# Kernel optimization log

Measured on AMD Instinct MI355X. Metric: run time of the kernel, lower is better.

## Reference

```python
import jax, jax.numpy as jnp
import numpy as np

B, T, C, H, DH, L, V = 4096, 32, 384, 6, 64, 6, 80


def _ln(x, g, b):
    m = x.mean(-1, keepdims=True)
    v = ((x - m) ** 2).mean(-1, keepdims=True)
    return (x - m) / jnp.sqrt(v + 1e-5) * g + b


def setup_inputs() -> dict:
    key = jax.random.key(0)
    ks = jax.random.split(key, 12)
    n = lambda k, s: jax.random.normal(k, s, dtype=jnp.float32) * 0.02
    return dict(
        idx=jax.random.randint(ks[0], (B, T), 0, V),
        tok_emb=n(ks[1], (V, C)),
        pos_emb=n(ks[2], (T, C)),
        ln1_g=jnp.ones((L, C), jnp.float32), ln1_b=jnp.zeros((L, C), jnp.float32),
        Wq=n(ks[3], (L, H, C, DH)), Wk=n(ks[4], (L, H, C, DH)), Wv=n(ks[5], (L, H, C, DH)),
        Wo=n(ks[6], (L, C, C)), bo=jnp.zeros((L, C), jnp.float32),
        ln2_g=jnp.ones((L, C), jnp.float32), ln2_b=jnp.zeros((L, C), jnp.float32),
        W1=n(ks[7], (L, C, 4 * C)), b1=jnp.zeros((L, 4 * C), jnp.float32),
        W2=n(ks[8], (L, 4 * C, C)), b2=jnp.zeros((L, C), jnp.float32),
        lnf_g=jnp.ones((C,), jnp.float32), lnf_b=jnp.zeros((C,), jnp.float32),
        Wlm=n(ks[9], (C, V)), blm=jnp.zeros((V,), jnp.float32),
    )


def reference(idx, tok_emb, pos_emb, ln1_g, ln1_b, Wq, Wk, Wv, Wo, bo,
              ln2_g, ln2_b, W1, b1, W2, b2, lnf_g, lnf_b, Wlm, blm):
    # token + position embeddings
    x = tok_emb[idx] + pos_emb[None]  # [B, T, C]
    mask = jnp.tril(jnp.ones((T, T), dtype=bool))  # causal

    def block(x, p):
        l1g, l1b, wq, wk, wv, wo, b_o, l2g, l2b, w1, b_1, w2, b_2 = p
        h = _ln(x, l1g, l1b)
        q = jnp.einsum('btc,hcd->bhtd', h, wq)
        k = jnp.einsum('btc,hcd->bhtd', h, wk)
        v = jnp.einsum('btc,hcd->bhtd', h, wv)
        s = jnp.einsum('bhtd,bhsd->bhts', q, k) * (DH ** -0.5)
        s = jnp.where(mask, s, -jnp.inf)
        a = jax.nn.softmax(s, axis=-1)  # dropout is identity in eval
        o = jnp.einsum('bhts,bhsd->bhtd', a, v)
        o = o.transpose(0, 2, 1, 3).reshape(x.shape[0], T, C)  # concat heads
        x = x + o @ wo + b_o
        h2 = _ln(x, l2g, l2b)
        x = x + jax.nn.relu(h2 @ w1 + b_1) @ w2 + b_2
        return x, None

    params = (ln1_g, ln1_b, Wq, Wk, Wv, Wo, bo, ln2_g, ln2_b, W1, b1, W2, b2)
    x, _ = jax.lax.scan(block, x, params)
    x = _ln(x, lnf_g, lnf_b)
    return x @ Wlm + blm  # [B, T, V]
```

## Files before the change

### kernel.cpp

```cpp
#include <hip/hip_runtime.h>
#include <hip/hip_fp16.h>
#include <stdint.h>


typedef unsigned short u16;
typedef __bf16 bf16x8 __attribute__((ext_vector_type(8)));
typedef float f32x4 __attribute__((ext_vector_type(4)));
typedef float f32x4v __attribute__((ext_vector_type(4)));
typedef unsigned uint2v __attribute__((ext_vector_type(2)));

#define M_TOK 131072
#define CDIM  384
#define TT    32
#define HH    6
#define DHEAD 64
#define LLAY  6
#define VOCAB 80
#define FFDIM 1536
#define QKVN  1152

__device__ __forceinline__ float b2f(u16 v) {
    union { unsigned int u; float f; } x; x.u = ((unsigned int)v) << 16; return x.f;
}
__device__ __forceinline__ u16 f2b(float f) {
    union { float f; unsigned int u; } x; x.f = f;
    unsigned int r = (x.u + 0x7fffu + ((x.u >> 16) & 1u)) >> 16;
    return (u16)r;
}
__device__ __forceinline__ void gload16(const u16* g, u16* l) {
    __builtin_amdgcn_global_load_lds(
        (const __attribute__((address_space(1))) void*)g,
        (__attribute__((address_space(3))) void*)l,
        16, 0, 0);
}
__device__ __forceinline__ float load_in(const void* p, size_t i, int m) {
    if (m == 0) return ((const float*)p)[i];
    u16 v = ((const u16*)p)[i];
    if (m == 1) return b2f(v);
    __half h; *(u16*)&h = v; return __half2float(h);
}

__global__ void detect_dtype_kernel(const void* ln1g, int* flag) {
    if (threadIdx.x == 0 && blockIdx.x == 0) {
        unsigned w = *(const unsigned*)ln1g;
        int m = 0;
        if (w == 0x3F803F80u) m = 1;
        else if (w == 0x3C003C00u) m = 2;
        *flag = m;
    }
}

__global__ void cvt_kernel(const void* __restrict__ src, u16* __restrict__ dst,
                           unsigned n, const int* __restrict__ flag) {
    const int m = *flag;
    unsigned i = blockIdx.x * 256 + threadIdx.x;
    if (i < n) dst[i] = f2b(load_in(src, i, m));
}

__global__ void transpose_kernel(const void* __restrict__ src, u16* __restrict__ dst,
                                 int R, int Cc, unsigned total,
                                 const int* __restrict__ flag) {
    const int m = *flag;
    unsigned i = blockIdx.x * 256 + threadIdx.x;
    if (i >= total) return;
    unsigned c  = i % R;
    unsigned t2 = i / R;
    unsigned n  = t2 % Cc;
    unsigned l  = t2 / Cc;
    dst[i] = f2b(load_in(src, ((size_t)l * R + c) * Cc + n, m));
}

__global__ void pack_qkv_kernel(const void* __restrict__ Wq, const void* __restrict__ Wk,
                                const void* __restrict__ Wv, u16* __restrict__ dst,
                                const int* __restrict__ flag) {
    const int m = *flag;
    unsigned i = blockIdx.x * 256 + threadIdx.x;
    const unsigned total = (unsigned)LLAY * QKVN * CDIM;
    if (i >= total) return;
    unsigned c  = i % CDIM;
    unsigned t2 = i / CDIM;
    unsigned n  = t2 % QKVN;
    unsigned l  = t2 / QKVN;
    const void* W = (n < 384) ? Wq : (n < 768) ? Wk : Wv;
    unsigned nn = n % 384;
    unsigned hh = nn >> 6, d = nn & 63;
    dst[i] = f2b(load_in(W, (((size_t)l * HH + hh) * CDIM + c) * DHEAD + d, m));
}

__global__ void embed_kernel(const int* __restrict__ idx, const void* __restrict__ tok,
                             const void* __restrict__ pos, float* __restrict__ x,
                             unsigned rows0, const int* __restrict__ flag) {
    const int m = *flag;
    unsigned i = blockIdx.x * 256 + threadIdx.x;
    unsigned c  = i % CDIM;
    unsigned bt = i / CDIM + rows0;
    unsigned t  = bt & (TT - 1);
    int id = idx[bt];
    x[i] = load_in(tok, (size_t)id * CDIM + c, m) + load_in(pos, (size_t)t * CDIM + c, m);
}

__global__ __launch_bounds__(256) void ln_kernel(const float* __restrict__ x,
                                                 const u16* __restrict__ g,
                                                 const u16* __restrict__ b,
                                                 u16* __restrict__ out) {
    const unsigned row  = blockIdx.x * 4 + (threadIdx.x >> 6);
    const unsigned lane = threadIdx.x & 63;
    const float* xr = x + (size_t)row * CDIM;
    float v[6]; float s = 0.f, s2 = 0.f;
#pragma unroll
    for (int j = 0; j < 6; j++) { v[j] = xr[lane + j * 64]; s += v[j]; s2 += v[j] * v[j]; }
#pragma unroll
    for (int off = 32; off; off >>= 1) { s += __shfl_xor(s, off); s2 += __shfl_xor(s2, off); }
    float mean = s * (1.f / CDIM);
    float var  = fmaxf(s2 * (1.f / CDIM) - mean * mean, 0.f);
    float rstd = rsqrtf(var + 1e-5f);
    u16* orow = out + (size_t)row * CDIM;
#pragma unroll
    for (int j = 0; j < 6; j++) {
        unsigned c = lane + j * 64;
        orow[c] = f2b((v[j] - mean) * rstd * b2f(g[c]) + b2f(b[c]));
    }
}

template<bool BIAS, bool RELU, bool RESID, bool NBOUND, bool FOUT>
__global__ __launch_bounds__(256, 4)
void gemm_kernel(const u16* __restrict__ A, const u16* __restrict__ Bt,
                 const u16* __restrict__ bias, const float* resid,
                 u16* __restrict__ Cb, float* Cf,
                 int N, int K, int nt) {
    __shared__ __align__(16) u16 smem[16384];
    u16* As = smem;
    u16* Bs = smem + 8192;
    float* eps = (float*)smem;

    const int tid  = threadIdx.x;
    const int lane = tid & 63;
    const int w    = tid >> 6;
    const int quad = lane >> 4;
    const int l16  = lane & 15;
    const int wm = w >> 1, wn = w & 1;

    const int id = blockIdx.x;
    const int sgrp = id >> 3;
    const int mtile = (id & 7) + 8 * (sgrp / nt);
    const int ntile = sgrp % nt;
    const long m0 = (long)mtile * 128;
    const long n0 = (long)ntile * 128;

    const u16* Ag[4]; const u16* Bg[4];
    u16* ldsA[4]; u16* ldsB[4];
#pragma unroll
    for (int n = 0; n < 4; n++) {
        const int si  = w * 256 + n * 64 + lane;
        const int row = si >> 3;
        const int p   = si & 7;
        const int s   = p ^ (row & 7);
        Ag[n] = A + (size_t)(m0 + row) * K + s * 8;
        long brow = n0 + row;
        if (NBOUND) brow = brow < N ? brow : N - 1;
        Bg[n] = Bt + (size_t)brow * K + s * 8;
        ldsA[n] = As + (size_t)(w * 256 + n * 64) * 8;
        ldsB[n] = Bs + (size_t)(w * 256 + n * 64) * 8;
    }

    f32x4 acc[4][4];
#pragma unroll
    for (int i = 0; i < 4; i++)
#pragma unroll
        for (int j = 0; j < 4; j++) acc[i][j] = f32x4{0.f, 0.f, 0.f, 0.f};

    for (int k0 = 0; k0 < K; k0 += 64) {
        __syncthreads();
#pragma unroll
        for (int n = 0; n < 4; n++) gload16(Ag[n] + k0, ldsA[n]);
#pragma unroll
        for (int n = 0; n < 4; n++) gload16(Bg[n] + k0, ldsB[n]);
        __syncthreads();
#pragma unroll
        for (int k32 = 0; k32 < 2; k32++) {
            bf16x8 af[4], bfr[4];
#pragma unroll
            for (int i = 0; i < 4; i++) {
                const int row = wm * 64 + i * 16 + l16;
                const int p   = (k32 * 4 + quad) ^ (row & 7);
                af[i] = *(const bf16x8*)(&As[row * 64 + p * 8]);
            }
#pragma unroll
            for (int j = 0; j < 4; j++) {
                const int row = wn * 64 + j * 16 + l16;
                const int p   = (k32 * 4 + quad) ^ (row & 7);
                bfr[j] = *(const bf16x8*)(&Bs[row * 64 + p * 8]);
            }
#pragma unroll
            for (int i = 0; i < 4; i++)
#pragma unroll
                for (int j = 0; j < 4; j++)
                    acc[i][j] = __builtin_amdgcn_mfma_f32_16x16x32_bf16(af[i], bfr[j], acc[i][j], 0, 0, 0);
        }
    }

    float bv[4];
#pragma unroll
    for (int j = 0; j < 4; j++) {
        if (BIAS) {
            int col = (int)n0 + wn * 64 + j * 16 + l16;
            bv[j] = (!NBOUND || col < N) ? b2f(bias[col]) : 0.f;
        } else bv[j] = 0.f;
    }

#pragma unroll
    for (int hhf = 0; hhf < 2; hhf++) {
        __syncthreads();
        if (wm == hhf) {
#pragma unroll
            for (int i = 0; i < 4; i++)
#pragma unroll
                for (int j = 0; j < 4; j++) {
                    const int lr = i * 16 + quad * 4;
                    const int lc = wn * 64 + j * 16 + l16;
#pragma unroll
                    for (int r = 0; r < 4; r++) {
                        float v = acc[i][j][r] + bv[j];
                        if (RELU) v = fmaxf(v, 0.f);
                        eps[(lr + r) * 128 + lc] = v;
                    }
                }
        }
        __syncthreads();
        const long rowbase = m0 + hhf * 64;
        const int lrow0 = tid >> 5;
        const int c = (tid & 31) * 4;
#pragma unroll
        for (int p = 0; p < 8; p++) {
            const int lrow = p * 8 + lrow0;
            const long grow = rowbase + lrow;
            f32x4v v = *(const f32x4v*)&eps[lrow * 128 + c];
            if (RESID) {
                const f32x4v rv = *(const f32x4v*)&resid[grow * N + n0 + c];
                v = v + rv;
                __builtin_nontemporal_store(v, (f32x4v*)&Cf[grow * N + n0 + c]);
            } else if (FOUT) {
                if (!NBOUND || (int)n0 + c + 3 < N)
                    __builtin_nontemporal_store(v, (f32x4v*)&Cf[grow * N + n0 + c]);
            } else {
                if (!NBOUND || (int)n0 + c + 3 < N) {
                    uint2v pk;
                    pk.x = (unsigned)f2b(v.x) | ((unsigned)f2b(v.y) << 16);
                    pk.y = (unsigned)f2b(v.z) | ((unsigned)f2b(v.w) << 16);
                    __builtin_nontemporal_store(pk, (uint2v*)&Cb[grow * N + n0 + c]);
                }
            }
        }
    }
}

__global__ __launch_bounds__(256, 2) void attn_kernel(const u16* __restrict__ qkv,
                                                      u16* __restrict__ o) {
    __shared__ __align__(16) u16 alds[4 * 3840];
    const int w    = threadIdx.x >> 6;
    u16* Pl = alds + w * 3840;
    u16* VT = Pl + 1280;

    const int gw   = blockIdx.x * 4 + w;
    const int seq  = gw / HH;
    const int h    = gw - seq * HH;
    const int lane = threadIdx.x & 63;
    const int l16  = lane & 15;
    const int quad = lane >> 4;

    const u16* base = qkv + (size_t)seq * TT * QKVN;
    const u16* Qb = base + h * DHEAD;
    const u16* Kb = base + 384 + h * DHEAD;
    const u16* Vb = base + 768 + h * DHEAD;

    {
        const int s  = lane & 31;
        const int hf = lane >> 5;
#pragma unroll
        for (int c = 0; c < 4; c++) {
            uint4 v = *(const uint4*)(Vb + (size_t)s * QKVN + hf * 32 + c * 8);
            const u16* pv = (const u16*)&v;
#pragma unroll
            for (int j = 0; j < 8; j++) {
                const int d = hf * 32 + c * 8 + j;
                VT[d * 40 + s] = pv[j];
            }
        }
    }

    bf16x8 qf[2][2], kf[2][2];
#pragma unroll
    for (int ti = 0; ti < 2; ti++)
#pragma unroll
        for (int kt = 0; kt < 2; kt++)
            qf[ti][kt] = *(const bf16x8*)(Qb + (size_t)(ti * 16 + l16) * QKVN + kt * 32 + quad * 8);
#pragma unroll
    for (int si = 0; si < 2; si++)
#pragma unroll
        for (int kt = 0; kt < 2; kt++)
            kf[si][kt] = *(const bf16x8*)(Kb + (size_t)(si * 16 + l16) * QKVN + kt * 32 + quad * 8);

    f32x4 S00 = f32x4{0.f, 0.f, 0.f, 0.f};
    f32x4 S10 = f32x4{0.f, 0.f, 0.f, 0.f};
    f32x4 S11 = f32x4{0.f, 0.f, 0.f, 0.f};
#pragma unroll
    for (int kt = 0; kt < 2; kt++) {
        S00 = __builtin_amdgcn_mfma_f32_16x16x32_bf16(qf[0][kt], kf[0][kt], S00, 0, 0, 0);
        S10 = __builtin_amdgcn_mfma_f32_16x16x32_bf16(qf[1][kt], kf[0][kt], S10, 0, 0, 0);
        S11 = __builtin_amdgcn_mfma_f32_16x16x32_bf16(qf[1][kt], kf[1][kt], S11, 0, 0, 0);
    }

#pragma unroll
    for (int ti = 0; ti < 2; ti++) {
#pragma unroll
        for (int r = 0; r < 4; r++) {
            const int t = ti * 16 + quad * 4 + r;
            float v0 = (ti ? S10[r] : S00[r]) * 0.125f;
            if (l16 > t) v0 = -1e30f;
            float v1 = -1e30f;
            if (ti == 1) {
                v1 = S11[r] * 0.125f;
                if (16 + l16 > t) v1 = -1e30f;
            }
            float m = fmaxf(v0, v1);
#pragma unroll
            for (int k = 1; k < 16; k <<= 1) m = fmaxf(m, __shfl_xor(m, k));
            const float e0 = __expf(v0 - m);
            const float e1 = (ti == 1) ? __expf(v1 - m) : 0.f;
            float l = e0 + e1;
#pragma unroll
            for (int k = 1; k < 16; k <<= 1) l += __shfl_xor(l, k);
            const float inv = 1.f / l;
            Pl[t * 40 + l16]      = f2b(e0 * inv);
            Pl[t * 40 + 16 + l16] = f2b(e1 * inv);
        }
    }

    bf16x8 pf[2], vf[4];
#pragma unroll
    for (int ti = 0; ti < 2; ti++)
        pf[ti] = *(const bf16x8*)(&Pl[(ti * 16 + l16) * 40 + quad * 8]);
#pragma unroll
    for (int dt = 0; dt < 4; dt++)
        vf[dt] = *(const bf16x8*)(&VT[(dt * 16 + l16) * 40 + quad * 8]);

    u16* ob = o + ((size_t)seq * TT) * CDIM + h * DHEAD;
#pragma unroll
    for (int ti = 0; ti < 2; ti++) {
#pragma unroll
        for (int dt = 0; dt < 4; dt++) {
            f32x4 O2 = f32x4{0.f, 0.f, 0.f, 0.f};
            O2 = __builtin_amdgcn_mfma_f32_16x16x32_bf16(pf[ti], vf[dt], O2, 0, 0, 0);
#pragma unroll
            for (int r = 0; r < 4; r++) {
                const int t = ti * 16 + quad * 4 + r;
                ob[(size_t)t * CDIM + dt * 16 + l16] = f2b(O2[r]);
            }
        }
    }
}

extern "C" void kernel_launch(void* const* d_in, const int* in_sizes, int n_in,
                              void* d_out, int out_size, void* d_ws, size_t ws_size,
                              hipStream_t stream) {
    const int*  idx  = (const int*)d_in[0];
    const void* tok  = d_in[1];
    const void* pos  = d_in[2];
    const void* ln1g = d_in[3];
    const void* ln1b = d_in[4];
    const void* Wq   = d_in[5];
    const void* Wk   = d_in[6];
    const void* Wv   = d_in[7];
    const void* Wo   = d_in[8];
    const void* bo   = d_in[9];
    const void* ln2g = d_in[10];
    const void* ln2b = d_in[11];
    const void* W1   = d_in[12];
    const void* b1   = d_in[13];
    const void* W2   = d_in[14];
    const void* b2   = d_in[15];
    const void* lnfg = d_in[16];
    const void* lnfb = d_in[17];
    const void* Wlm  = d_in[18];
    const void* blm  = d_in[19];

    const size_t wq_b  = (size_t)LLAY * QKVN * CDIM * 2;
    const size_t wo_b  = (size_t)LLAY * CDIM * CDIM * 2;
    const size_t w1_b  = (size_t)LLAY * FFDIM * CDIM * 2;
    const size_t w2_b  = (size_t)LLAY * CDIM * FFDIM * 2;
    const size_t wlm_b = (size_t)VOCAB * CDIM * 2;
    const size_t wts   = wq_b + wo_b + w1_b + w2_b + wlm_b;

    const unsigned P_LN1G = 0,      P_LN1B = 2304,  P_BO  = 4608;
    const unsigned P_LN2G = 6912,   P_LN2B = 9216,  P_B1  = 11520;
    const unsigned P_B2   = 20736,  P_LNFG = 23040, P_LNFB = 23424;
    const unsigned P_BLM  = 23808,  P_TOT  = 23888;
    const size_t pbuf_b = ((size_t)P_TOT * 2 + 255) & ~(size_t)255;

    int NC = 32;
    {
        const int cand[6] = {1, 2, 4, 8, 16, 32};
        for (int ci = 0; ci < 6; ci++) {
            size_t rows_c = (size_t)M_TOK / cand[ci];
            size_t need = rows_c * 5376 + wts + pbuf_b + 4096;
            if (need <= ws_size) { NC = cand[ci]; break; }
        }
    }
    const size_t rows = (size_t)M_TOK / NC;
    const int mt = (int)(rows / 128);

    char* ws = (char*)d_ws;
    size_t off = 0;
    float* x    = (float*)(ws + off); off += rows * CDIM * 4;
    u16*   h    = (u16*)(ws + off);   off += rows * CDIM * 2;
    char*  S    = ws + off;           off += rows * 3072;
    u16*   qkv  = (u16*)S;
    u16*   o    = (u16*)(S + rows * QKVN * 2);
    u16*   u    = (u16*)S;
    u16* wqkvT  = (u16*)(ws + off);   off += wq_b;
    u16* woT    = (u16*)(ws + off);   off += wo_b;
    u16* w1T    = (u16*)(ws + off);   off += w1_b;
    u16* w2T    = (u16*)(ws + off);   off += w2_b;
    u16* wlmT   = (u16*)(ws + off);   off += wlm_b;
    u16* pbuf   = (u16*)(ws + off);   off += pbuf_b;
    int* flag   = (int*)(ws + off);   off += 256;

    detect_dtype_kernel<<<1, 64, 0, stream>>>(ln1g, flag);

    struct { const void* src; unsigned doff, n; } cv[10] = {
        { ln1g, P_LN1G, 2304 }, { ln1b, P_LN1B, 2304 }, { bo, P_BO, 2304 },
        { ln2g, P_LN2G, 2304 }, { ln2b, P_LN2B, 2304 }, { b1, P_B1, 9216 },
        { b2,   P_B2,   2304 }, { lnfg, P_LNFG, 384 },  { lnfb, P_LNFB, 384 },
        { blm,  P_BLM,  80 },
    };
    for (int i = 0; i < 10; i++)
        cvt_kernel<<<(cv[i].n + 255) / 256, 256, 0, stream>>>(cv[i].src, pbuf + cv[i].doff, cv[i].n, flag);

    {
        unsigned tq = (unsigned)LLAY * QKVN * CDIM;
        pack_qkv_kernel<<<(tq + 255) / 256, 256, 0, stream>>>(Wq, Wk, Wv, wqkvT, flag);
        unsigned t1 = (unsigned)LLAY * CDIM * CDIM;
        transpose_kernel<<<(t1 + 255) / 256, 256, 0, stream>>>(Wo, woT, CDIM, CDIM, t1, flag);
        unsigned t2t = (unsigned)LLAY * CDIM * FFDIM;
        transpose_kernel<<<(t2t + 255) / 256, 256, 0, stream>>>(W1, w1T, CDIM, FFDIM, t2t, flag);
        transpose_kernel<<<(t2t + 255) / 256, 256, 0, stream>>>(W2, w2T, FFDIM, CDIM, t2t, flag);
        unsigned t3 = (unsigned)VOCAB * CDIM;
        transpose_kernel<<<(t3 + 255) / 256, 256, 0, stream>>>(Wlm, wlmT, CDIM, VOCAB, t3, flag);
    }

    for (int c = 0; c < NC; c++) {
        const size_t r0 = c * rows;
        embed_kernel<<<(rows * CDIM) / 256, 256, 0, stream>>>(idx, tok, pos, x, (unsigned)r0, flag);

        for (int l = 0; l < LLAY; l++) {
            ln_kernel<<<rows / 4, 256, 0, stream>>>(x, pbuf + P_LN1G + l * CDIM, pbuf + P_LN1B + l * CDIM, h);
            gemm_kernel<false, false, false, false, false><<<mt * (QKVN / 128), 256, 0, stream>>>(
                h, wqkvT + (size_t)l * QKVN * CDIM, nullptr, nullptr, qkv, nullptr, QKVN, CDIM, QKVN / 128);
            attn_kernel<<<(rows / TT) * HH / 4, 256, 0, stream>>>(qkv, o);
            gemm_kernel<true, false, true, false, false><<<mt * (CDIM / 128), 256, 0, stream>>>(
                o, woT + (size_t)l * CDIM * CDIM, pbuf + P_BO + l * CDIM, x, nullptr, x, CDIM, CDIM, CDIM / 128);
            ln_kernel<<<rows / 4, 256, 0, stream>>>(x, pbuf + P_LN2G + l * CDIM, pbuf + P_LN2B + l * CDIM, h);
            gemm_kernel<true, true, false, false, false><<<mt * (FFDIM / 128), 256, 0, stream>>>(
                h, w1T + (size_t)l * FFDIM * CDIM, pbuf + P_B1 + l * FFDIM, nullptr, u, nullptr, FFDIM, CDIM, FFDIM / 128);
            gemm_kernel<true, false, true, false, false><<<mt * (CDIM / 128), 256, 0, stream>>>(
                u, w2T + (size_t)l * CDIM * FFDIM, pbuf + P_B2 + l * CDIM, x, nullptr, x, CDIM, FFDIM, CDIM / 128);
        }

        ln_kernel<<<rows / 4, 256, 0, stream>>>(x, pbuf + P_LNFG, pbuf + P_LNFB, h);
        gemm_kernel<true, false, false, true, true><<<mt, 256, 0, stream>>>(
            h, wlmT, pbuf + P_BLM, nullptr, nullptr, (float*)d_out + r0 * VOCAB, VOCAB, CDIM, 1);
    }
}
```

Baseline: 5.933 ms.

## Double-buffer LDS tiles in GEMM and remap block-to-tile ordering

The GEMM main loop now uses two LDS buffers, issuing global-to-LDS loads for the next K tile while MFMA runs on the current one, with one barrier per iteration instead of two. LDS use doubles to 64 KB and launch bounds drop from 4 to 2 blocks per SM. Block-to-tile mapping also changes: block index is split into 8 contiguous chunks across the grid rather than interleaving 8 M-tiles per group, which alters L2 reuse of weight tiles. The risks are lower occupancy and the loss of the prior tile grouping's cache locality.

```diff
diff --git a/kernel.cpp b/kernel.cpp
--- a/kernel.cpp
+++ b/kernel.cpp
@@ -123,14 +123,12 @@
 }
 
 template<bool BIAS, bool RELU, bool RESID, bool NBOUND, bool FOUT>
-__global__ __launch_bounds__(256, 4)
+__global__ __launch_bounds__(256, 2)
 void gemm_kernel(const u16* __restrict__ A, const u16* __restrict__ Bt,
                  const u16* __restrict__ bias, const float* resid,
                  u16* __restrict__ Cb, float* Cf,
                  int N, int K, int nt) {
-    __shared__ __align__(16) u16 smem[16384];
-    u16* As = smem;
-    u16* Bs = smem + 8192;
+    __shared__ __align__(16) u16 smem[32768];
     float* eps = (float*)smem;
 
     const int tid  = threadIdx.x;
@@ -140,10 +138,10 @@
     const int l16  = lane & 15;
     const int wm = w >> 1, wn = w & 1;
 
-    const int id = blockIdx.x;
-    const int sgrp = id >> 3;
-    const int mtile = (id & 7) + 8 * (sgrp / nt);
-    const int ntile = sgrp % nt;
+    const int per = gridDim.x >> 3;
+    const int id  = (blockIdx.x & 7) * per + (blockIdx.x >> 3);
+    const int mtile = id / nt;
+    const int ntile = id - mtile * nt;
     const long m0 = (long)mtile * 128;
     const long n0 = (long)ntile * 128;
 
@@ -159,8 +157,8 @@
         long brow = n0 + row;
         if (NBOUND) brow = brow < N ? brow : N - 1;
         Bg[n] = Bt + (size_t)brow * K + s * 8;
-        ldsA[n] = As + (size_t)(w * 256 + n * 64) * 8;
-        ldsB[n] = Bs + (size_t)(w * 256 + n * 64) * 8;
+        ldsA[n] = smem + (size_t)(w * 256 + n * 64) * 8;
+        ldsB[n] = smem + 8192 + (size_t)(w * 256 + n * 64) * 8;
     }
 
     f32x4 acc[4][4];
@@ -169,13 +167,27 @@
 #pragma unroll
         for (int j = 0; j < 4; j++) acc[i][j] = f32x4{0.f, 0.f, 0.f, 0.f};
 
-    for (int k0 = 0; k0 < K; k0 += 64) {
-        __syncthreads();
-#pragma unroll
-        for (int n = 0; n < 4; n++) gload16(Ag[n] + k0, ldsA[n]);
-#pragma unroll
-        for (int n = 0; n < 4; n++) gload16(Bg[n] + k0, ldsB[n]);
-        __syncthreads();
+    const int KT = K >> 6;
+
+#pragma unroll
+    for (int n = 0; n < 4; n++) gload16(Ag[n], ldsA[n]);
+#pragma unroll
+    for (int n = 0; n < 4; n++) gload16(Bg[n], ldsB[n]);
+    __syncthreads();
+
+    int cur = 0;
+    for (int t = 0; t < KT; t++) {
+        const int nxt = cur ^ 1;
+        if (t + 1 < KT) {
+            const int k0 = (t + 1) << 6;
+            const int bo = nxt << 14;
+#pragma unroll
+            for (int n = 0; n < 4; n++) gload16(Ag[n] + k0, ldsA[n] + bo);
+#pragma unroll
+            for (int n = 0; n < 4; n++) gload16(Bg[n] + k0, ldsB[n] + bo);
+        }
+        const u16* As = smem + (cur << 14);
+        const u16* Bs = As + 8192;
 #pragma unroll
         for (int k32 = 0; k32 < 2; k32++) {
             bf16x8 af[4], bfr[4];
@@ -197,6 +209,8 @@
                 for (int j = 0; j < 4; j++)
                     acc[i][j] = __builtin_amdgcn_mfma_f32_16x16x32_bf16(af[i], bfr[j], acc[i][j], 0, 0, 0);
         }
+        __syncthreads();
+        cur = nxt;
     }
 
     float bv[4];
```

Measured after the change: 6.253 ms. 1.05x slower.

## Retile GEMMs to 512-thread blocks with 128x256 wide tiles for QKV/FFN1

Applied to the files above, without the earlier changes.

The GEMM kernel now runs 8 waves per block. It uses a 128x256 output tile for the QKV and FFN1 projections and 128x128 for the others. The QKV GEMM gets 5 N-tiles with bounds clamping, since 1152 is not a multiple of 256. The wider tile is meant to raise A-tile reuse and cut the number of blocks and A reloads. The cost is more LDS per block, more epilogue phases, and about 11% wasted compute on the padded QKV tile.

```diff
diff --git a/kernel.cpp b/kernel.cpp
--- a/kernel.cpp
+++ b/kernel.cpp
@@ -122,13 +122,17 @@
     }
 }
 
-template<bool BIAS, bool RELU, bool RESID, bool NBOUND, bool FOUT>
-__global__ __launch_bounds__(256, 4)
+template<bool WIDE, bool BIAS, bool RELU, bool RESID, bool NBOUND, bool FOUT>
+__global__ __launch_bounds__(512, WIDE ? 4 : 6)
 void gemm_kernel(const u16* __restrict__ A, const u16* __restrict__ Bt,
                  const u16* __restrict__ bias, const float* resid,
                  u16* __restrict__ Cb, float* Cf,
                  int N, int K, int nt) {
-    __shared__ __align__(16) u16 smem[16384];
+    constexpr int BN = WIDE ? 256 : 128;
+    constexpr int NF = WIDE ? 4 : 2;
+    constexpr int WC = BN / 4;
+    constexpr int BI = BN / 64;
+    __shared__ __align__(16) u16 smem[8192 + BN * 64];
     u16* As = smem;
     u16* Bs = smem + 8192;
     float* eps = (float*)smem;
@@ -138,47 +142,54 @@
     const int w    = tid >> 6;
     const int quad = lane >> 4;
     const int l16  = lane & 15;
-    const int wm = w >> 1, wn = w & 1;
+    const int wm = w >> 2, wn = w & 3;
 
     const int id = blockIdx.x;
     const int sgrp = id >> 3;
     const int mtile = (id & 7) + 8 * (sgrp / nt);
     const int ntile = sgrp % nt;
     const long m0 = (long)mtile * 128;
-    const long n0 = (long)ntile * 128;
-
-    const u16* Ag[4]; const u16* Bg[4];
-    u16* ldsA[4]; u16* ldsB[4];
-#pragma unroll
-    for (int n = 0; n < 4; n++) {
-        const int si  = w * 256 + n * 64 + lane;
+    const long n0 = (long)ntile * BN;
+
+    const u16* Ag[2]; u16* ldsA[2];
+    const u16* Bg[BI]; u16* ldsB[BI];
+#pragma unroll
+    for (int n = 0; n < 2; n++) {
+        const int si  = w * 128 + n * 64 + lane;
         const int row = si >> 3;
         const int p   = si & 7;
         const int s   = p ^ (row & 7);
         Ag[n] = A + (size_t)(m0 + row) * K + s * 8;
+        ldsA[n] = As + (size_t)(w * 128 + n * 64) * 8;
+    }
+#pragma unroll
+    for (int n = 0; n < BI; n++) {
+        const int si  = (w * BI + n) * 64 + lane;
+        const int row = si >> 3;
+        const int p   = si & 7;
+        const int s   = p ^ (row & 7);
         long brow = n0 + row;
         if (NBOUND) brow = brow < N ? brow : N - 1;
         Bg[n] = Bt + (size_t)brow * K + s * 8;
-        ldsA[n] = As + (size_t)(w * 256 + n * 64) * 8;
-        ldsB[n] = Bs + (size_t)(w * 256 + n * 64) * 8;
-    }
-
-    f32x4 acc[4][4];
+        ldsB[n] = Bs + (size_t)((w * BI + n) * 64) * 8;
+    }
+
+    f32x4 acc[4][NF];
 #pragma unroll
     for (int i = 0; i < 4; i++)
 #pragma unroll
-        for (int j = 0; j < 4; j++) acc[i][j] = f32x4{0.f, 0.f, 0.f, 0.f};
+        for (int j = 0; j < NF; j++) acc[i][j] = f32x4{0.f, 0.f, 0.f, 0.f};
 
     for (int k0 = 0; k0 < K; k0 += 64) {
         __syncthreads();
 #pragma unroll
-        for (int n = 0; n < 4; n++) gload16(Ag[n] + k0, ldsA[n]);
-#pragma unroll
-        for (int n = 0; n < 4; n++) gload16(Bg[n] + k0, ldsB[n]);
+        for (int n = 0; n < 2; n++)  gload16(Ag[n] + k0, ldsA[n]);
+#pragma unroll
+        for (int n = 0; n < BI; n++) gload16(Bg[n] + k0, ldsB[n]);
         __syncthreads();
 #pragma unroll
         for (int k32 = 0; k32 < 2; k32++) {
-            bf16x8 af[4], bfr[4];
+            bf16x8 af[4], bfr[NF];
 #pragma unroll
             for (int i = 0; i < 4; i++) {
                 const int row = wm * 64 + i * 16 + l16;
@@ -186,68 +197,77 @@
                 af[i] = *(const bf16x8*)(&As[row * 64 + p * 8]);
             }
 #pragma unroll
-            for (int j = 0; j < 4; j++) {
-                const int row = wn * 64 + j * 16 + l16;
+            for (int j = 0; j < NF; j++) {
+                const int row = wn * WC + j * 16 + l16;
                 const int p   = (k32 * 4 + quad) ^ (row & 7);
                 bfr[j] = *(const bf16x8*)(&Bs[row * 64 + p * 8]);
             }
 #pragma unroll
             for (int i = 0; i < 4; i++)
 #pragma unroll
-                for (int j = 0; j < 4; j++)
+                for (int j = 0; j < NF; j++)
                     acc[i][j] = __builtin_amdgcn_mfma_f32_16x16x32_bf16(af[i], bfr[j], acc[i][j], 0, 0, 0);
         }
     }
 
-    float bv[4];
-#pragma unroll
-    for (int j = 0; j < 4; j++) {
+    float bv[NF];
+#pragma unroll
+    for (int j = 0; j < NF; j++) {
         if (BIAS) {
-            int col = (int)n0 + wn * 64 + j * 16 + l16;
+            int col = (int)n0 + wn * WC + j * 16 + l16;
             bv[j] = (!NBOUND || col < N) ? b2f(bias[col]) : 0.f;
         } else bv[j] = 0.f;
     }
 
-#pragma unroll
-    for (int hhf = 0; hhf < 2; hhf++) {
+    constexpr int SR  = WIDE ? 32 : 64;
+    constexpr int NPH = 128 / SR;
+    constexpr int IB  = SR / 16;
+    constexpr int TPR = BN / 4;
+    constexpr int RPP = 512 / TPR;
+    const int cc = (tid & (TPR - 1)) * 4;
+    const int rr = tid / TPR;
+#pragma unroll
+    for (int q = 0; q < NPH; q++) {
         __syncthreads();
-        if (wm == hhf) {
-#pragma unroll
-            for (int i = 0; i < 4; i++)
-#pragma unroll
-                for (int j = 0; j < 4; j++) {
-                    const int lr = i * 16 + quad * 4;
-                    const int lc = wn * 64 + j * 16 + l16;
+        if (wm == (q * SR) / 64) {
+            const int ibase = ((q * SR) % 64) / 16;
+#pragma unroll
+            for (int ii = 0; ii < IB; ii++)
+#pragma unroll
+                for (int j = 0; j < NF; j++) {
+                    const int lr = ii * 16 + quad * 4;
+                    const int lc = wn * WC + j * 16 + l16;
 #pragma unroll
                     for (int r = 0; r < 4; r++) {
-                        float v = acc[i][j][r] + bv[j];
+                        float v = acc[ibase + ii][j][r] + bv[j];
                         if (RELU) v = fmaxf(v, 0.f);
-                        eps[(lr + r) * 128 + lc] = v;
+                        eps[(lr + r) * BN + lc] = v;
                     }
                 }
         }
         __syncthreads();
-        const long rowbase = m0 + hhf * 64;
-        const int lrow0 = tid >> 5;
-        const int c = (tid & 31) * 4;
-#pragma unroll
-        for (int p = 0; p < 8; p++) {
-            const int lrow = p * 8 + lrow0;
+        const long rowbase = m0 + q * SR;
+#pragma unroll
+        for (int p = 0; p < SR / RPP; p++) {
+            const int lrow = p * RPP + rr;
             const long grow = rowbase + lrow;
-            f32x4v v = *(const f32x4v*)&eps[lrow * 128 + c];
+            f32x4v v = *(const f32x4v*)&eps[lrow * BN + cc];
+            const long col = n0 + cc;
             if (RESID) {
-                const f32x4v rv = *(const f32x4v*)&resid[grow * N + n0 + c];
-                v = v + rv;
-                __builtin_nontemporal_store(v, (f32x4v*)&Cf[grow * N + n0 + c]);
+                if (!NBOUND || col + 3 < N) {
+                    const f32x4v rv = *(const f32x4v*)&resid[grow * N + col];
+                    v = v + rv;
+                    __builtin_nontemporal_store(v, (f32x4v*)&Cf[grow * N + col]);
+                }
             } else if (FOUT) {
-                if (!NBOUND || (int)n0 + c + 3 < N)
-                    __builtin_nontemporal_store(v, (f32x4v*)&Cf[grow * N + n0 + c]);
+                if (!NBOUND || col + 3 < N)
+                    __builtin_nontemporal_store(v, (f32x4v*)&Cf[grow * N + col]);
             } else {
-                if (!NBOUND || (int)n0 + c + 3 < N) {
+                if (!NBOUND || col + 3 < N) {
                     uint2v pk;
                     pk.x = (unsigned)f2b(v.x) | ((unsigned)f2b(v.y) << 16);
                     pk.y = (unsigned)f2b(v.z) | ((unsigned)f2b(v.w) << 16);
-                    __builtin_nontemporal_store(pk, (uint2v*)&Cb[grow * N + n0 + c]);
+                    __builtin_nontemporal_store(pk, (uint2v*)&Cb[grow * N + col]);
                 }
             }
         }
@@ -454,20 +474,20 @@
 
         for (int l = 0; l < LLAY; l++) {
             ln_kernel<<<rows / 4, 256, 0, stream>>>(x, pbuf + P_LN1G + l * CDIM, pbuf + P_LN1B + l * CDIM, h);
-            gemm_kernel<false, false, false, false, false><<<mt * (QKVN / 128), 256, 0, stream>>>(
-                h, wqkvT + (size_t)l * QKVN * CDIM, nullptr, nullptr, qkv, nullptr, QKVN, CDIM, QKVN / 128);
+            gemm_kernel<true, false, false, false, true, false><<<mt * 5, 512, 0, stream>>>(
+                h, wqkvT + (size_t)l * QKVN * CDIM, nullptr, nullptr, qkv, nullptr, QKVN, CDIM, 5);
             attn_kernel<<<(rows / TT) * HH / 4, 256, 0, stream>>>(qkv, o);
-            gemm_kernel<true, false, true, false, false><<<mt * (CDIM / 128), 256, 0, stream>>>(
-                o, woT + (size_t)l * CDIM * CDIM, pbuf + P_BO + l * CDIM, x, nullptr, x, CDIM, CDIM, CDIM / 128);
+            gemm_kernel<false, true, false, true, false, false><<<mt * 3, 512, 0, stream>>>(
+                o, woT + (size_t)l * CDIM * CDIM, pbuf + P_BO + l * CDIM, x, nullptr, x, CDIM, CDIM, 3);
             ln_kernel<<<rows / 4, 256, 0, stream>>>(x, pbuf + P_LN2G + l * CDIM, pbuf + P_LN2B + l * CDIM, h);
-            gemm_kernel<true, true, false, false, false><<<mt * (FFDIM / 128), 256, 0, stream>>>(
-                h, w1T + (size_t)l * FFDIM * CDIM, pbuf + P_B1 + l * FFDIM, nullptr, u, nullptr, FFDIM, CDIM, FFDIM / 128);
-            gemm_kernel<true, false, true, false, false><<<mt * (CDIM / 128), 256, 0, stream>>>(
-                u, w2T + (size_t)l * CDIM * FFDIM, pbuf + P_B2 + l * CDIM, x, nullptr, x, CDIM, FFDIM, CDIM / 128);
+            gemm_kernel<true, true, true, false, false, false><<<mt * 6, 512, 0, stream>>>(
+                h, w1T + (size_t)l * FFDIM * CDIM, pbuf + P_B1 + l * FFDIM, nullptr, u, nullptr, FFDIM, CDIM, 6);
+            gemm_kernel<false, true, false, true, false, false><<<mt * 3, 512, 0, stream>>>(
+                u, w2T + (size_t)l * CDIM * FFDIM, pbuf + P_B2 + l * CDIM, x, nullptr, x, CDIM, FFDIM, 3);
         }
 
         ln_kernel<<<rows / 4, 256, 0, stream>>>(x, pbuf + P_LNFG, pbuf + P_LNFB, h);
-        gemm_kernel<true, false, false, true, true><<<mt, 256, 0, stream>>>(
+        gemm_kernel<false, true, false, false, true, true><<<mt, 512, 0, stream>>>(
             h, wlmT, pbuf + P_BLM, nullptr, nullptr, (float*)d_out + r0 * VOCAB, VOCAB, CDIM, 1);
     }
 }
```

Measured after the change: 5.872 ms. No clear change (-1.0%).
